# Kernel tuning notes

Hardware: AMD Instinct MI355X
Metric: run time of the kernel (lower is better)

The kernel has to match this reference:

```python
import jax, jax.numpy as jnp
import numpy as np

B, N, L, E, U, G, R, C = 128, 50000, 8, 250000, 10000, 20000, 2000, 2


def setup_inputs() -> dict:
    key = jax.random.key(0)
    k1, k2, k3, k4, k5, k6 = jax.random.split(key, 6)
    rng = np.random.default_rng(0)
    # unique index sets (scatter .set requires unique targets for determinism)
    gene_map = jnp.asarray(rng.permutation(N)[:G].astype(np.int64))
    dst_unique = jnp.asarray(np.stack([rng.permutation(N)[:U] for _ in range(L)]).astype(np.int64))
    root_ids = jnp.asarray(rng.permutation(N)[:R].astype(np.int64))
    return {
        "X_gene_batch": jax.random.normal(k1, (B, G), dtype=jnp.float32),
        "layer_weight": 0.01 * jnp.ones((L,), dtype=jnp.float32),
        "node_bias": 0.1 * jax.random.normal(k2, (N,), dtype=jnp.float32),
        "head_W": jax.random.normal(k3, (C, R), dtype=jnp.float32) / np.sqrt(R),
        "head_b": jnp.zeros((C,), dtype=jnp.float32),
        "gene_map": gene_map,
        "src": jax.random.randint(k4, (L, E), 0, N, dtype=jnp.int64),
        "dst_pos": jax.random.randint(k5, (L, E), 0, U, dtype=jnp.int64),
        "dst_unique": dst_unique,
        "root_ids": root_ids,
    }


def reference(X_gene_batch, layer_weight, node_bias, head_W, head_b,
              gene_map, src, dst_pos, dst_unique, root_ids):
    B_, dtype = X_gene_batch.shape[0], X_gene_batch.dtype
    N_ = node_bias.shape[0]
    L_, _ = src.shape
    U_ = dst_unique.shape[1]
    # init scalar state: h[:, gene_map] = X
    h = jnp.zeros((B_, N_), dtype=dtype).at[:, gene_map].set(X_gene_batch)
    for li in range(L_):  # small fixed layer loop (structurally distinct steps)
        msg = h[:, src[li]] * layer_weight[li]                      # [B, E] gather + scale
        agg = jnp.zeros((B_, U_), dtype=dtype).at[:, dst_pos[li]].add(msg)  # segment sum
        h_dst = jnp.tanh(agg + node_bias[dst_unique[li]][None, :])  # bias + tanh (dropout=0)
        h = h.at[:, dst_unique[li]].set(h_dst)                      # scatter write back
    feat = h[:, root_ids]                                           # [B, R] roots concat
    return feat @ head_W.T + head_b                                 # [B, C]
```

## Files before the change

### kernel.cpp

```cpp
#include <hip/hip_runtime.h>

constexpr int Bb = 128;
constexpr int Nn = 50000;
constexpr int Ll = 8;
constexpr int Ee = 250000;
constexpr int Uu = 10000;
constexpr int Gg = 20000;
constexpr int Rr = 2000;
constexpr int Cc = 2;

constexpr int NB1 = 40;
constexpr int BW1 = 256;
constexpr int CAP = 7424;
constexpr int CH2 = 256;
constexpr int RIT = Uu * 32;
constexpr int NSTG = 7;

typedef __attribute__((ext_vector_type(2))) float f32x2;


__device__ __forceinline__ float b2f(unsigned short x) {
    return __uint_as_float((unsigned)x << 16);
}
__device__ __forceinline__ unsigned short f2b(float f) {
    unsigned u = __float_as_uint(f);
    return (unsigned short)((u + 0x7FFFu + ((u >> 16) & 1u)) >> 16);
}
__device__ __forceinline__ unsigned pkbf(float a, float b) {
    return (unsigned)f2b(a) | ((unsigned)f2b(b) << 16);
}

__global__ void zero_kernel(unsigned int* __restrict__ hz, unsigned int* __restrict__ h8z,
                            unsigned int* __restrict__ pz, int* __restrict__ gcur) {
    int idx = blockIdx.x * blockDim.x + threadIdx.x;
    if (idx < Nn * 64) hz[idx] = 0u;
    if (idx < Nn * 32) h8z[idx] = 0u;
    if (idx < Ll * Nn / 2) pz[idx] = 0xFFFFFFFFu;
    if (idx < Ll * NB1) gcur[idx] = 0;
}

__global__ __launch_bounds__(256) void genes_kernel(const float* __restrict__ X,
                                                    const int* __restrict__ gmap,
                                                    const int* __restrict__ dstu,
                                                    unsigned short* __restrict__ h,
                                                    unsigned int* __restrict__ h8,
                                                    unsigned short* __restrict__ postab) {
    int gt = blockIdx.x * 256 + (int)threadIdx.x;
    if (gt < Ll * Uu) {
        int li = gt / Uu;
        postab[(size_t)li * Nn + dstu[gt]] = (unsigned short)(gt - li * Uu);
    }
    int g0 = blockIdx.x * 32;
    __shared__ float tile[32][129];
    #pragma unroll
    for (int i = 0; i < 16; ++i) {
        int idx = i * 256 + (int)threadIdx.x;
        int gl = idx & 31, b = idx >> 5;
        tile[gl][b] = X[(size_t)b * Gg + g0 + gl];
    }
    __syncthreads();
    #pragma unroll
    for (int i = 0; i < 16; ++i) {
        int idx = i * 256 + (int)threadIdx.x;
        int b = idx & 127, gl = idx >> 7;
        h[(size_t)gmap[g0 + gl] * Bb + b] = f2b(tile[gl][b]);
    }
    #pragma unroll
    for (int i = 0; i < 4; ++i) {
        int idx = i * 256 + (int)threadIdx.x;
        int q = idx & 31, gl = idx >> 5;
        int node = gmap[g0 + gl];
        int w8 = __builtin_amdgcn_cvt_pk_fp8_f32(tile[gl][q * 4 + 0], tile[gl][q * 4 + 1], 0, false);
        w8 = __builtin_amdgcn_cvt_pk_fp8_f32(tile[gl][q * 4 + 2], tile[gl][q * 4 + 3], w8, true);
        h8[(size_t)node * 32 + q] = (unsigned int)w8;
    }
}

__global__ void rowof_kernel(const unsigned short* __restrict__ postab,
                             unsigned int* __restrict__ rowof) {
    int n = blockIdx.x * 256 + (int)threadIdx.x;
    if (n >= Nn) return;
    unsigned r = (unsigned)n;
    rowof[n] = r;
    #pragma unroll
    for (int li = 1; li < Ll; ++li) {
        unsigned short p = postab[(size_t)(li - 1) * Nn + n];
        if (p != 0xFFFFu) r = (unsigned)(Nn + (li - 1) * Uu + (int)p);
        rowof[(size_t)li * Nn + n] = r;
    }
}

__global__ __launch_bounds__(256) void part_kernel(const int* __restrict__ src,
                                                   const int* __restrict__ dstp,
                                                   int* __restrict__ gcur,
                                                   unsigned int* __restrict__ region) {
    int li = blockIdx.x / CH2, ch = blockIdx.x % CH2;
    const int ePer = (Ee + CH2 - 1) / CH2;
    int e0 = ch * ePer, e1 = min(e0 + ePer, Ee);
    const int* s = src + (size_t)li * Ee;
    const int* d = dstp + (size_t)li * Ee;

    __shared__ int hist[NB1];
    __shared__ int base[NB1];
    __shared__ int cur[NB1];
    if (threadIdx.x < NB1) { hist[threadIdx.x] = 0; cur[threadIdx.x] = 0; }
    __syncthreads();

    for (int e = e0 + (int)threadIdx.x; e < e1; e += 256)
        atomicAdd(&hist[d[e] >> 8], 1);
    __syncthreads();

    if (threadIdx.x < NB1) {
        int c = hist[threadIdx.x];
        base[threadIdx.x] = (c > 0) ? atomicAdd(&gcur[li * NB1 + (int)threadIdx.x], c) : 0;
    }
    __syncthreads();

    for (int e = e0 + (int)threadIdx.x; e < e1; e += 256) {
        int dd = d[e];
        int bkt = dd >> 8;
        unsigned int packed = ((unsigned int)s[e] << 8) | (unsigned int)(dd & 255);
        int pos = base[bkt] + atomicAdd(&cur[bkt], 1);
        region[((size_t)li * NB1 + bkt) * CAP + pos] = packed;
    }
}

__global__ __launch_bounds__(256) void emit_kernel(const unsigned int* __restrict__ region,
                                                   const int* __restrict__ gcur,
                                                   const unsigned int* __restrict__ rowof,
                                                   unsigned int* __restrict__ ssrc,
                                                   int* __restrict__ rp) {
    int li = blockIdx.x / NB1, b = blockIdx.x % NB1;
    int n = gcur[li * NB1 + b];
    const unsigned int* r = region + ((size_t)li * NB1 + b) * CAP;
    __shared__ int hh[BW1];
    __shared__ int ofs[BW1];
    __shared__ int sbase;
    __shared__ unsigned short lout[CAP];
    if (threadIdx.x < BW1) hh[threadIdx.x] = 0;
    if (threadIdx.x < 64) {
        int t = threadIdx.x;
        int v = (t < NB1) ? gcur[li * NB1 + t] : 0;
        int sc = v;
        #pragma unroll
        for (int off = 1; off < 64; off <<= 1) {
            int x = __shfl_up(sc, (unsigned)off, 64);
            if (t >= off) sc += x;
        }
        if (t == b) sbase = sc - v;
        if (b == NB1 - 1 && t == NB1 - 1) rp[li * (Uu + 1) + Uu] = sc;
    }
    __syncthreads();
    for (int i = threadIdx.x; i < n; i += 256) atomicAdd(&hh[r[i] & 255], 1);
    __syncthreads();
    if (threadIdx.x < 64) {
        int carry = 0;
        #pragma unroll
        for (int c = 0; c < BW1 / 64; ++c) {
            int v = hh[c * 64 + (int)threadIdx.x];
            int sc = v;
            #pragma unroll
            for (int off = 1; off < 64; off <<= 1) {
                int x = __shfl_up(sc, (unsigned)off, 64);
                if ((int)threadIdx.x >= off) sc += x;
            }
            ofs[c * 64 + (int)threadIdx.x] = carry + sc - v;
            carry += __shfl(sc, 63, 64);
        }
    }
    __syncthreads();
    int base = sbase;
    if (threadIdx.x < BW1) {
        int dg = b * BW1 + (int)threadIdx.x;
        if (dg < Uu) rp[li * (Uu + 1) + dg] = base + ofs[threadIdx.x];
    }
    __syncthreads();
    for (int i = threadIdx.x; i < n; i += 256) {
        unsigned int p = r[i];
        int pos = atomicAdd(&ofs[p & 255], 1);
        lout[pos] = (unsigned short)(p >> 8);
    }
    __syncthreads();
    unsigned int* o = ssrc + (size_t)li * Ee + base;
    const unsigned int* ro = rowof + (size_t)li * Nn;
    for (int i = threadIdx.x; i < n; i += 256) o[i] = ro[lout[i]];
}

__global__ __launch_bounds__(256) void layer_kernel(unsigned short* __restrict__ h,
                                                    unsigned int* __restrict__ h8,
                                                    const unsigned int* __restrict__ ssrc,
                                                    const int* __restrict__ rp,
                                                    const int* __restrict__ dstu,
                                                    const float* __restrict__ lw,
                                                    const float* __restrict__ bias,
                                                    int li) {
    int idx = blockIdx.x * 256 + (int)threadIdx.x;
    if (idx >= RIT) return;
    int u = idx >> 5;
    int lane5 = idx & 31;
    int sub = lane5 >> 3;
    int l8 = lane5 & 7;
    int beg = rp[u], end = rp[u + 1];
    const uint4* hp = (const uint4*)h8;
    float acc[16];
    #pragma unroll
    for (int j = 0; j < 16; ++j) acc[j] = 0.f;
    f32x2 p;
    int k = beg + sub;
    for (; k + 4 < end; k += 8) {
        unsigned s0 = ssrc[k], s1 = ssrc[k + 4];
        uint4 v0 = hp[(size_t)s0 * 8 + l8];
        uint4 v1 = hp[(size_t)s1 * 8 + l8];
        p = __builtin_amdgcn_cvt_pk_f32_fp8(v0.x, false); acc[0] += p.x;  acc[1] += p.y;
        p = __builtin_amdgcn_cvt_pk_f32_fp8(v0.x, true);  acc[2] += p.x;  acc[3] += p.y;
        p = __builtin_amdgcn_cvt_pk_f32_fp8(v0.y, false); acc[4] += p.x;  acc[5] += p.y;
        p = __builtin_amdgcn_cvt_pk_f32_fp8(v0.y, true);  acc[6] += p.x;  acc[7] += p.y;
        p = __builtin_amdgcn_cvt_pk_f32_fp8(v0.z, false); acc[8] += p.x;  acc[9] += p.y;
        p = __builtin_amdgcn_cvt_pk_f32_fp8(v0.z, true);  acc[10] += p.x; acc[11] += p.y;
        p = __builtin_amdgcn_cvt_pk_f32_fp8(v0.w, false); acc[12] += p.x; acc[13] += p.y;
        p = __builtin_amdgcn_cvt_pk_f32_fp8(v0.w, true);  acc[14] += p.x; acc[15] += p.y;
        p = __builtin_amdgcn_cvt_pk_f32_fp8(v1.x, false); acc[0] += p.x;  acc[1] += p.y;
        p = __builtin_amdgcn_cvt_pk_f32_fp8(v1.x, true);  acc[2] += p.x;  acc[3] += p.y;
        p = __builtin_amdgcn_cvt_pk_f32_fp8(v1.y, false); acc[4] += p.x;  acc[5] += p.y;
        p = __builtin_amdgcn_cvt_pk_f32_fp8(v1.y, true);  acc[6] += p.x;  acc[7] += p.y;
        p = __builtin_amdgcn_cvt_pk_f32_fp8(v1.z, false); acc[8] += p.x;  acc[9] += p.y;
        p = __builtin_amdgcn_cvt_pk_f32_fp8(v1.z, true);  acc[10] += p.x; acc[11] += p.y;
        p = __builtin_amdgcn_cvt_pk_f32_fp8(v1.w, false); acc[12] += p.x; acc[13] += p.y;
        p = __builtin_amdgcn_cvt_pk_f32_fp8(v1.w, true);  acc[14] += p.x; acc[15] += p.y;
    }
    if (k < end) {
        uint4 v0 = hp[(size_t)ssrc[k] * 8 + l8];
        p = __builtin_amdgcn_cvt_pk_f32_fp8(v0.x, false); acc[0] += p.x;  acc[1] += p.y;
        p = __builtin_amdgcn_cvt_pk_f32_fp8(v0.x, true);  acc[2] += p.x;  acc[3] += p.y;
        p = __builtin_amdgcn_cvt_pk_f32_fp8(v0.y, false); acc[4] += p.x;  acc[5] += p.y;
        p = __builtin_amdgcn_cvt_pk_f32_fp8(v0.y, true);  acc[6] += p.x;  acc[7] += p.y;
        p = __builtin_amdgcn_cvt_pk_f32_fp8(v0.z, false); acc[8] += p.x;  acc[9] += p.y;
        p = __builtin_amdgcn_cvt_pk_f32_fp8(v0.z, true);  acc[10] += p.x; acc[11] += p.y;
        p = __builtin_amdgcn_cvt_pk_f32_fp8(v0.w, false); acc[12] += p.x; acc[13] += p.y;
        p = __builtin_amdgcn_cvt_pk_f32_fp8(v0.w, true);  acc[14] += p.x; acc[15] += p.y;
    }
    #pragma unroll
    for (int j = 0; j < 16; ++j) {
        acc[j] += __shfl_xor(acc[j], 8, 64);
        acc[j] += __shfl_xor(acc[j], 16, 64);
    }
    if (sub == 0) {
        float wv = lw[li];
        int node = dstu[li * Uu + u];
        float bs = bias[node];
        float t[16];
        #pragma unroll
        for (int j = 0; j < 16; ++j) t[j] = tanhf(acc[j] * wv + bs);
        uint4 o0, o1;
        o0.x = pkbf(t[0], t[1]);   o0.y = pkbf(t[2], t[3]);
        o0.z = pkbf(t[4], t[5]);   o0.w = pkbf(t[6], t[7]);
        o1.x = pkbf(t[8], t[9]);   o1.y = pkbf(t[10], t[11]);
        o1.z = pkbf(t[12], t[13]); o1.w = pkbf(t[14], t[15]);
        *(uint4*)(h + (size_t)node * Bb + l8 * 16) = o0;
        *(uint4*)(h + (size_t)node * Bb + l8 * 16 + 8) = o1;
        if (li < NSTG) {
            uint4 of;
            int w8;
            w8 = __builtin_amdgcn_cvt_pk_fp8_f32(t[0], t[1], 0, false);
            w8 = __builtin_amdgcn_cvt_pk_fp8_f32(t[2], t[3], w8, true);   of.x = (unsigned)w8;
            w8 = __builtin_amdgcn_cvt_pk_fp8_f32(t[4], t[5], 0, false);
            w8 = __builtin_amdgcn_cvt_pk_fp8_f32(t[6], t[7], w8, true);   of.y = (unsigned)w8;
            w8 = __builtin_amdgcn_cvt_pk_fp8_f32(t[8], t[9], 0, false);
            w8 = __builtin_amdgcn_cvt_pk_fp8_f32(t[10], t[11], w8, true); of.z = (unsigned)w8;
            w8 = __builtin_amdgcn_cvt_pk_fp8_f32(t[12], t[13], 0, false);
            w8 = __builtin_amdgcn_cvt_pk_fp8_f32(t[14], t[15], w8, true); of.w = (unsigned)w8;
            *(uint4*)(h8 + (size_t)(Nn + li * Uu + u) * 32 + l8 * 4) = of;
        }
    }
}

__global__ void head_kernel(const unsigned short* __restrict__ h,
                            const int* __restrict__ roots,
                            const float* __restrict__ W, const float* __restrict__ hb,
                            float* __restrict__ out) {
    int b = blockIdx.x;
    int t = threadIdx.x;
    float a0 = 0.f, a1 = 0.f;
    for (int r = t; r < Rr; r += 256) {
        float v = b2f(h[(size_t)roots[r] * Bb + b]);
        a0 += v * W[r];
        a1 += v * W[Rr + r];
    }
    __shared__ float s0[256], s1[256];
    s0[t] = a0; s1[t] = a1;
    __syncthreads();
    for (int off = 128; off > 0; off >>= 1) {
        if (t < off) { s0[t] += s0[t + off]; s1[t] += s1[t + off]; }
        __syncthreads();
    }
    if (t == 0) {
        out[b * Cc + 0] = s0[0] + hb[0];
        out[b * Cc + 1] = s1[0] + hb[1];
    }
}

extern "C" void kernel_launch(void* const* d_in, const int* in_sizes, int n_in,
                              void* d_out, int out_size, void* d_ws, size_t ws_size,
                              hipStream_t stream) {
    const float* X      = (const float*)d_in[0];
    const float* lw     = (const float*)d_in[1];
    const float* bias   = (const float*)d_in[2];
    const float* headW  = (const float*)d_in[3];
    const float* headb  = (const float*)d_in[4];
    const int*   gmap   = (const int*)d_in[5];
    const int*   src    = (const int*)d_in[6];
    const int*   dstp   = (const int*)d_in[7];
    const int*   dstu   = (const int*)d_in[8];
    const int*   roots  = (const int*)d_in[9];
    float* out = (float*)d_out;

    char* w = (char*)d_ws;
    unsigned short* h_t    = (unsigned short*)w; w += (size_t)Nn * Bb * 2;
    unsigned int*   h8     = (unsigned int*)w;   w += (size_t)(Nn + NSTG * Uu) * Bb;
    unsigned int*   region = (unsigned int*)w;   w += (size_t)Ll * NB1 * CAP * 4;
    unsigned int*   ssrc   = (unsigned int*)w;   w += (size_t)Ll * Ee * 4;
    int*            rp     = (int*)w;            w += (size_t)Ll * (Uu + 1) * 4;
    unsigned short* postab = (unsigned short*)w; w += (size_t)Ll * Nn * 2;
    unsigned int*   rowof  = (unsigned int*)w;   w += (size_t)Ll * Nn * 4;
    int*            gcur   = (int*)w;            w += (size_t)Ll * NB1 * 4;

    const int BLK = 256;

    zero_kernel<<<(Nn * 64 + BLK - 1) / BLK, BLK, 0, stream>>>(
        (unsigned int*)h_t, h8, (unsigned int*)postab, gcur);
    genes_kernel<<<Gg / 32, BLK, 0, stream>>>(X, gmap, dstu, h_t, h8, postab);
    rowof_kernel<<<(Nn + BLK - 1) / BLK, BLK, 0, stream>>>(postab, rowof);

    part_kernel<<<Ll * CH2, BLK, 0, stream>>>(src, dstp, gcur, region);
    emit_kernel<<<Ll * NB1, BLK, 0, stream>>>(region, gcur, rowof, ssrc, rp);

    for (int li = 0; li < Ll; ++li) {
        layer_kernel<<<(RIT + BLK - 1) / BLK, BLK, 0, stream>>>(
            h_t, h8, ssrc + (size_t)li * Ee, rp + (size_t)li * (Uu + 1),
            dstu, lw, bias, li);
    }

    head_kernel<<<Bb, 256, 0, stream>>>(h_t, roots, headW, headb, out);
}
```

Baseline: 143.2 us.

## Only zero and write bf16 state for root nodes; merge genes and partition kernels

Adds a per-node root bitmap so the full bf16 hidden-state buffer no longer needs zeroing, and layer kernels store bf16 outputs only for nodes the head reads. The genes init and edge partition work are fused into a single launch with block-range dispatch. This cuts memset bandwidth, layer store traffic and one launch, at the cost of an extra byte load per output and a larger combined kernel.

Result: faster. 135.8 us (-5.2%).

```diff
diff --git a/kernel.cpp b/kernel.cpp
--- a/kernel.cpp
+++ b/kernel.cpp
@@ -15,6 +15,7 @@
 constexpr int CH2 = 256;
 constexpr int RIT = Uu * 32;
 constexpr int NSTG = 7;
+constexpr int GB  = Gg / 32;
 
 typedef __attribute__((ext_vector_type(2))) float f32x2;
 
@@ -31,48 +32,84 @@
 }
 
 __global__ void zero_kernel(unsigned int* __restrict__ hz, unsigned int* __restrict__ h8z,
-                            unsigned int* __restrict__ pz, int* __restrict__ gcur) {
+                            unsigned int* __restrict__ pz, int* __restrict__ gcur,
+                            unsigned char* __restrict__ rbit, const int* __restrict__ roots) {
     int idx = blockIdx.x * blockDim.x + threadIdx.x;
-    if (idx < Nn * 64) hz[idx] = 0u;
     if (idx < Nn * 32) h8z[idx] = 0u;
     if (idx < Ll * Nn / 2) pz[idx] = 0xFFFFFFFFu;
+    if (idx < Rr * 64) {
+        int r = idx >> 6, wv = idx & 63;
+        hz[(size_t)roots[r] * 64 + wv] = 0u;
+    }
+    if (idx < Nn) rbit[idx] = 0;
     if (idx < Ll * NB1) gcur[idx] = 0;
 }
 
-__global__ __launch_bounds__(256) void genes_kernel(const float* __restrict__ X,
-                                                    const int* __restrict__ gmap,
-                                                    const int* __restrict__ dstu,
-                                                    unsigned short* __restrict__ h,
-                                                    unsigned int* __restrict__ h8,
-                                                    unsigned short* __restrict__ postab) {
-    int gt = blockIdx.x * 256 + (int)threadIdx.x;
-    if (gt < Ll * Uu) {
-        int li = gt / Uu;
-        postab[(size_t)li * Nn + dstu[gt]] = (unsigned short)(gt - li * Uu);
-    }
-    int g0 = blockIdx.x * 32;
+__global__ __launch_bounds__(256) void genes_part_kernel(
+        const float* __restrict__ X, const int* __restrict__ gmap,
+        const int* __restrict__ dstu, const int* __restrict__ roots,
+        unsigned short* __restrict__ h, unsigned int* __restrict__ h8,
+        unsigned short* __restrict__ postab, unsigned char* __restrict__ rbit,
+        const int* __restrict__ src, const int* __restrict__ dstp,
+        int* __restrict__ gcur, unsigned int* __restrict__ region) {
     __shared__ float tile[32][129];
-    #pragma unroll
-    for (int i = 0; i < 16; ++i) {
-        int idx = i * 256 + (int)threadIdx.x;
-        int gl = idx & 31, b = idx >> 5;
-        tile[gl][b] = X[(size_t)b * Gg + g0 + gl];
-    }
-    __syncthreads();
-    #pragma unroll
-    for (int i = 0; i < 16; ++i) {
-        int idx = i * 256 + (int)threadIdx.x;
-        int b = idx & 127, gl = idx >> 7;
-        h[(size_t)gmap[g0 + gl] * Bb + b] = f2b(tile[gl][b]);
-    }
-    #pragma unroll
-    for (int i = 0; i < 4; ++i) {
-        int idx = i * 256 + (int)threadIdx.x;
-        int q = idx & 31, gl = idx >> 5;
-        int node = gmap[g0 + gl];
-        int w8 = __builtin_amdgcn_cvt_pk_fp8_f32(tile[gl][q * 4 + 0], tile[gl][q * 4 + 1], 0, false);
-        w8 = __builtin_amdgcn_cvt_pk_fp8_f32(tile[gl][q * 4 + 2], tile[gl][q * 4 + 3], w8, true);
-        h8[(size_t)node * 32 + q] = (unsigned int)w8;
+    if (blockIdx.x < GB) {
+        int gt = blockIdx.x * 256 + (int)threadIdx.x;
+        if (gt < Ll * Uu) {
+            int li = gt / Uu;
+            postab[(size_t)li * Nn + dstu[gt]] = (unsigned short)(gt - li * Uu);
+        }
+        if (gt < Rr) rbit[roots[gt]] = 1;
+        int g0 = blockIdx.x * 32;
+        #pragma unroll
+        for (int i = 0; i < 16; ++i) {
+            int idx = i * 256 + (int)threadIdx.x;
+            int gl = idx & 31, b = idx >> 5;
+            tile[gl][b] = X[(size_t)b * Gg + g0 + gl];
+        }
+        __syncthreads();
+        #pragma unroll
+        for (int i = 0; i < 16; ++i) {
+            int idx = i * 256 + (int)threadIdx.x;
+            int b = idx & 127, gl = idx >> 7;
+            h[(size_t)gmap[g0 + gl] * Bb + b] = f2b(tile[gl][b]);
+        }
+        #pragma unroll
+        for (int i = 0; i < 4; ++i) {
+            int idx = i * 256 + (int)threadIdx.x;
+            int q = idx & 31, gl = idx >> 5;
+            int node = gmap[g0 + gl];
+            int w8 = __builtin_amdgcn_cvt_pk_fp8_f32(tile[gl][q * 4 + 0], tile[gl][q * 4 + 1], 0, false);
+            w8 = __builtin_amdgcn_cvt_pk_fp8_f32(tile[gl][q * 4 + 2], tile[gl][q * 4 + 3], w8, true);
+            h8[(size_t)node * 32 + q] = (unsigned int)w8;
+        }
+    } else {
+        int pb = blockIdx.x - GB;
+        int li = pb / CH2, ch = pb % CH2;
+        const int ePer = (Ee + CH2 - 1) / CH2;
+        int e0 = ch * ePer, e1 = min(e0 + ePer, Ee);
+        const int* s = src + (size_t)li * Ee;
+        const int* d = dstp + (size_t)li * Ee;
+        int* hist = (int*)&tile[0][0];
+        int* base = hist + NB1;
+        int* cur  = base + NB1;
+        if (threadIdx.x < NB1) { hist[threadIdx.x] = 0; cur[threadIdx.x] = 0; }
+        __syncthreads();
+        for (int e = e0 + (int)threadIdx.x; e < e1; e += 256)
+            atomicAdd(&hist[d[e] >> 8], 1);
+        __syncthreads();
+        if (threadIdx.x < NB1) {
+            int c = hist[threadIdx.x];
+            base[threadIdx.x] = (c > 0) ? atomicAdd(&gcur[li * NB1 + (int)threadIdx.x], c) : 0;
+        }
+        __syncthreads();
+        for (int e = e0 + (int)threadIdx.x; e < e1; e += 256) {
+            int dd = d[e];
+            int bkt = dd >> 8;
+            unsigned int packed = ((unsigned int)s[e] << 8) | (unsigned int)(dd & 255);
+            int pos = base[bkt] + atomicAdd(&cur[bkt], 1);
+            region[((size_t)li * NB1 + bkt) * CAP + pos] = packed;
+        }
     }
 }
 
@@ -87,41 +124,6 @@
         unsigned short p = postab[(size_t)(li - 1) * Nn + n];
         if (p != 0xFFFFu) r = (unsigned)(Nn + (li - 1) * Uu + (int)p);
         rowof[(size_t)li * Nn + n] = r;
-    }
-}
-
-__global__ __launch_bounds__(256) void part_kernel(const int* __restrict__ src,
-                                                   const int* __restrict__ dstp,
-                                                   int* __restrict__ gcur,
-                                                   unsigned int* __restrict__ region) {
-    int li = blockIdx.x / CH2, ch = blockIdx.x % CH2;
-    const int ePer = (Ee + CH2 - 1) / CH2;
-    int e0 = ch * ePer, e1 = min(e0 + ePer, Ee);
-    const int* s = src + (size_t)li * Ee;
-    const int* d = dstp + (size_t)li * Ee;
-
-    __shared__ int hist[NB1];
-    __shared__ int base[NB1];
-    __shared__ int cur[NB1];
-    if (threadIdx.x < NB1) { hist[threadIdx.x] = 0; cur[threadIdx.x] = 0; }
-    __syncthreads();
-
-    for (int e = e0 + (int)threadIdx.x; e < e1; e += 256)
-        atomicAdd(&hist[d[e] >> 8], 1);
-    __syncthreads();
-
-    if (threadIdx.x < NB1) {
-        int c = hist[threadIdx.x];
-        base[threadIdx.x] = (c > 0) ? atomicAdd(&gcur[li * NB1 + (int)threadIdx.x], c) : 0;
-    }
-    __syncthreads();
-
-    for (int e = e0 + (int)threadIdx.x; e < e1; e += 256) {
-        int dd = d[e];
-        int bkt = dd >> 8;
-        unsigned int packed = ((unsigned int)s[e] << 8) | (unsigned int)(dd & 255);
-        int pos = base[bkt] + atomicAdd(&cur[bkt], 1);
-        region[((size_t)li * NB1 + bkt) * CAP + pos] = packed;
     }
 }
 
@@ -193,6 +195,7 @@
                                                     const int* __restrict__ dstu,
                                                     const float* __restrict__ lw,
                                                     const float* __restrict__ bias,
+                                                    const unsigned char* __restrict__ rbit,
                                                     int li) {
     int idx = blockIdx.x * 256 + (int)threadIdx.x;
     if (idx >= RIT) return;
@@ -251,13 +254,15 @@
         float t[16];
         #pragma unroll
         for (int j = 0; j < 16; ++j) t[j] = tanhf(acc[j] * wv + bs);
-        uint4 o0, o1;
-        o0.x = pkbf(t[0], t[1]);   o0.y = pkbf(t[2], t[3]);
-        o0.z = pkbf(t[4], t[5]);   o0.w = pkbf(t[6], t[7]);
-        o1.x = pkbf(t[8], t[9]);   o1.y = pkbf(t[10], t[11]);
-        o1.z = pkbf(t[12], t[13]); o1.w = pkbf(t[14], t[15]);
-        *(uint4*)(h + (size_t)node * Bb + l8 * 16) = o0;
-        *(uint4*)(h + (size_t)node * Bb + l8 * 16 + 8) = o1;
+        if (rbit[node]) {
+            uint4 o0, o1;
+            o0.x = pkbf(t[0], t[1]);   o0.y = pkbf(t[2], t[3]);
+            o0.z = pkbf(t[4], t[5]);   o0.w = pkbf(t[6], t[7]);
+            o1.x = pkbf(t[8], t[9]);   o1.y = pkbf(t[10], t[11]);
+            o1.z = pkbf(t[12], t[13]); o1.w = pkbf(t[14], t[15]);
+            *(uint4*)(h + (size_t)node * Bb + l8 * 16) = o0;
+            *(uint4*)(h + (size_t)node * Bb + l8 * 16 + 8) = o1;
+        }
         if (li < NSTG) {
             uint4 of;
             int w8;
@@ -323,21 +328,23 @@
     unsigned short* postab = (unsigned short*)w; w += (size_t)Ll * Nn * 2;
     unsigned int*   rowof  = (unsigned int*)w;   w += (size_t)Ll * Nn * 4;
     int*            gcur   = (int*)w;            w += (size_t)Ll * NB1 * 4;
+    unsigned char*  rbit   = (unsigned char*)w;  w += (size_t)((Nn + 63) & ~63);
 
     const int BLK = 256;
 
-    zero_kernel<<<(Nn * 64 + BLK - 1) / BLK, BLK, 0, stream>>>(
-        (unsigned int*)h_t, h8, (unsigned int*)postab, gcur);
-    genes_kernel<<<Gg / 32, BLK, 0, stream>>>(X, gmap, dstu, h_t, h8, postab);
+    zero_kernel<<<(Nn * 32 + BLK - 1) / BLK, BLK, 0, stream>>>(
+        (unsigned int*)h_t, h8, (unsigned int*)postab, gcur, rbit, roots);
+
+    genes_part_kernel<<<GB + Ll * CH2, BLK, 0, stream>>>(
+        X, gmap, dstu, roots, h_t, h8, postab, rbit, src, dstp, gcur, region);
+
     rowof_kernel<<<(Nn + BLK - 1) / BLK, BLK, 0, stream>>>(postab, rowof);
-
-    part_kernel<<<Ll * CH2, BLK, 0, stream>>>(src, dstp, gcur, region);
     emit_kernel<<<Ll * NB1, BLK, 0, stream>>>(region, gcur, rowof, ssrc, rp);
 
     for (int li = 0; li < Ll; ++li) {
         layer_kernel<<<(RIT + BLK - 1) / BLK, BLK, 0, stream>>>(
             h_t, h8, ssrc + (size_t)li * Ee, rp + (size_t)li * (Uu + 1),
-            dstu, lw, bias, li);
+            dstu, lw, bias, rbit, li);
     }
 
     head_kernel<<<Bb, 256, 0, stream>>>(h_t, roots, headW, headb, out);
```
